# Kernel tuning notes

Hardware: AMD Instinct MI355X
Metric: run time of the kernel (lower is better)

The kernel has to match this reference:

```python
import jax, jax.numpy as jnp
import numpy as np

B, S, D, R = 4, 4096, 1024, 128
EPS_MAG = 1e-8
EPS_LN = 1e-5


def setup_inputs() -> dict:
    key = jax.random.key(0)
    ks = jax.random.split(key, 24)
    w = lambda k, shape, s=0.02: (jax.random.normal(k, shape, jnp.float32) * s)
    d = {}
    d["x"] = jax.random.normal(ks[0], (B, S, D), jnp.float32)
    d["W_dt_down"] = w(ks[1], (D, R))            # dt_proj_down (no bias)
    d["W_dt_up"] = w(ks[2], (R, D))
    d["b_dt_up"] = jnp.full((D,), -4.0, jnp.float32)  # nn.init.constant_(-4.0)
    d["W_gate"] = w(ks[3], (D, D)); d["b_gate"] = jnp.zeros((D,), jnp.float32)
    d["W_phi1"] = w(ks[4], (D, D)); d["b_phi1"] = jnp.zeros((D,), jnp.float32)
    d["W_phi2"] = w(ks[5], (D, D)); d["b_phi2"] = jnp.zeros((D,), jnp.float32)
    d["omega_base"] = jax.random.normal(ks[6], (D,), jnp.float32) * 0.1
    d["W_omega"] = w(ks[7], (D, D)); d["b_omega"] = jnp.zeros((D,), jnp.float32)
    d["W_mag"] = w(ks[8], (D, D)); d["b_mag"] = jnp.zeros((D,), jnp.float32)
    d["W_qoff"] = w(ks[9], (D, D)); d["b_qoff"] = jnp.zeros((D,), jnp.float32)
    d["ln_g"] = jnp.ones((2 * D,), jnp.float32); d["ln_b"] = jnp.zeros((2 * D,), jnp.float32)
    d["W_out1"] = w(ks[10], (2 * D, D)); d["b_out1"] = jnp.zeros((D,), jnp.float32)
    d["W_out2"] = w(ks[11], (D, D)); d["b_out2"] = jnp.zeros((D,), jnp.float32)
    return d


def _forward(x, W_dt_down, W_dt_up, b_dt_up, W_gate, b_gate, W_phi1, b_phi1,
             W_phi2, b_phi2, omega_base, W_omega, b_omega, W_mag, b_mag,
             W_qoff, b_qoff, ln_g, ln_b, W_out1, b_out1, W_out2, b_out2):
    h = x  # expand_factor == 1 -> in_proj is Identity
    # input-dependent delta (low-rank)
    dt = jax.nn.softplus((h @ W_dt_down) @ W_dt_up + b_dt_up)        # [B,S,D]
    select_gate = jax.nn.sigmoid(h @ W_gate + b_gate)
    omega = omega_base + (h @ W_omega + b_omega)
    omega_scaled = omega * dt * 0.01
    phi_init = jax.nn.gelu(h @ W_phi1 + b_phi1, approximate=False) @ W_phi2 + b_phi2
    phi = phi_init + jnp.cumsum(omega_scaled, axis=1)                # phase accumulation
    magnitude = jax.nn.sigmoid(h @ W_mag + b_mag) * 5.0
    content = select_gate * h * magnitude
    memory_real = jnp.cumsum(content * jnp.cos(phi), axis=1)
    memory_imag = jnp.cumsum(content * jnp.sin(phi), axis=1)
    acc_mag = jnp.cumsum(magnitude * select_gate, axis=1)
    sqrt_mag = jnp.sqrt(acc_mag + EPS_MAG)
    mr = memory_real / sqrt_mag
    mi = memory_imag / sqrt_mag
    # rotation-based retrieval
    phi_q = phi + (h @ W_qoff + b_qoff)
    cq, sq = jnp.cos(phi_q), jnp.sin(phi_q)
    retrieved_real = mr * cq + mi * sq
    retrieved_imag = mi * cq - mr * sq
    ctx = jnp.concatenate([retrieved_real, retrieved_imag], axis=-1)  # [B,S,2D]
    mu = jnp.mean(ctx, axis=-1, keepdims=True)
    var = jnp.mean((ctx - mu) ** 2, axis=-1, keepdims=True)
    ln = (ctx - mu) / jnp.sqrt(var + EPS_LN) * ln_g + ln_b
    out = jax.nn.gelu(ln @ W_out1 + b_out1, approximate=False) @ W_out2 + b_out2
    return x + out


def reference(x, W_dt_down, W_dt_up, b_dt_up, W_gate, b_gate, W_phi1, b_phi1,
              W_phi2, b_phi2, omega_base, W_omega, b_omega, W_mag, b_mag,
              W_qoff, b_qoff, ln_g, ln_b, W_out1, b_out1, W_out2, b_out2):
    return _forward(x, W_dt_down, W_dt_up, b_dt_up, W_gate, b_gate, W_phi1, b_phi1,
                    W_phi2, b_phi2, omega_base, W_omega, b_omega, W_mag, b_mag,
                    W_qoff, b_qoff, ln_g, ln_b, W_out1, b_out1, W_out2, b_out2)
```

## Files before the change

### kernel.cpp

```cpp
#include <hip/hip_runtime.h>


#define D_ 1024
#define S_ 4096
#define MH 8192
#define CHUNK 64

typedef float f32x4 __attribute__((ext_vector_type(4)));
typedef __bf16 bf16x8 __attribute__((ext_vector_type(8)));
typedef short s16x8 __attribute__((ext_vector_type(8)));

typedef __attribute__((address_space(1))) void gvoid;
typedef __attribute__((address_space(3))) void lvoid;

__device__ __forceinline__ void g2l16(const void* g, void* l) {
  __builtin_amdgcn_global_load_lds((gvoid*)g, (lvoid*)l, 16, 0, 0);
}

__device__ __forceinline__ float bflo(unsigned int w){ union{unsigned int i; float f;} c; c.i = w<<16; return c.f; }
__device__ __forceinline__ float bfhi(unsigned int w){ union{unsigned int i; float f;} c; c.i = w & 0xFFFF0000u; return c.f; }
__device__ __forceinline__ unsigned short f2bf(float f){
  union{float f; unsigned int i;} c; c.f=f;
  unsigned int u = c.i + 0x7FFFu + ((c.i>>16)&1u);
  return (unsigned short)(u>>16);
}
__device__ __forceinline__ unsigned int pack2(float lo, float hi){
  return (unsigned int)f2bf(lo) | ((unsigned int)f2bf(hi)<<16);
}

__device__ __forceinline__ float sig_(float x){ return 1.f/(1.f+__expf(-x)); }
__device__ __forceinline__ float gelu_(float x){ return 0.5f*x*(1.f+erff(x*0.70710678118654752440f)); }
__device__ __forceinline__ float softplus_(float x){ return (x>0.f) ? x + log1pf(__expf(-x)) : log1pf(__expf(x)); }

template<int EPI, int KK>
__global__ __launch_bounds__(256)
void gemmH(const unsigned short* __restrict__ A,
           const unsigned short* __restrict__ Bt,
           const float* __restrict__ bias,
           const float* __restrict__ extra,
           unsigned short* __restrict__ out0,
           float* __restrict__ outf)
{
  __shared__ unsigned short As[2][128*32];
  __shared__ unsigned short Bs[2][128*32];
  const int tid = threadIdx.x;
  const int m0 = blockIdx.x * 128;
  const int n0 = blockIdx.y * 128;
  const int lane = tid & 63;
  const int wv = tid >> 6;
  const int wr = wv >> 1, wc = wv & 1;
  const int fr = lane & 15, fg = lane >> 4;

  const int r0 = tid >> 2;
  const int k8 = (tid & 3) * 8;

  const unsigned short* ArowA = A  + (size_t)(m0+r0)*KK + k8;
  const unsigned short* ArowB = A  + (size_t)(m0+r0+64)*KK + k8;
  const unsigned short* BrowA = Bt + (size_t)(n0+r0)*KK + k8;
  const unsigned short* BrowB = Bt + (size_t)(n0+r0+64)*KK + k8;

  f32x4 acc[4][4];
#pragma unroll
  for (int i=0;i<4;i++)
#pragma unroll
    for (int j=0;j<4;j++)
#pragma unroll
      for (int q=0;q<4;q++) acc[i][j][q] = 0.f;

  auto STAGE = [&](int buf, int t) {
    const int k0 = t << 5;
    g2l16(ArowA + k0, &As[buf][(size_t)tid*8]);
    g2l16(ArowB + k0, &As[buf][(size_t)(tid+256)*8]);
    g2l16(BrowA + k0, &Bs[buf][(size_t)tid*8]);
    g2l16(BrowB + k0, &Bs[buf][(size_t)(tid+256)*8]);
  };
  auto COMPUTE = [&](int buf) {
    s16x8 af[4], bfr[4];
#pragma unroll
    for (int mf=0; mf<4; mf++) af[mf]  = *(const s16x8*)&As[buf][(wr*64 + mf*16 + fr)*32 + fg*8];
#pragma unroll
    for (int nf=0; nf<4; nf++) bfr[nf] = *(const s16x8*)&Bs[buf][(wc*64 + nf*16 + fr)*32 + fg*8];
#pragma unroll
    for (int mf=0; mf<4; mf++)
#pragma unroll
      for (int nf=0; nf<4; nf++)
        acc[mf][nf] = __builtin_amdgcn_mfma_f32_16x16x32_bf16(
          __builtin_bit_cast(bf16x8, af[mf]), __builtin_bit_cast(bf16x8, bfr[nf]),
          acc[mf][nf], 0, 0, 0);
  };

  const int nt = KK >> 5;
  STAGE(0, 0);
  STAGE(1, 1);
  int cur = 0;
  for (int t = 0; t < nt - 1; ++t) {
    asm volatile("s_waitcnt vmcnt(4)" ::: "memory");
    __builtin_amdgcn_s_barrier();
    __builtin_amdgcn_sched_barrier(0);
    COMPUTE(cur);
    __builtin_amdgcn_s_barrier();
    __builtin_amdgcn_sched_barrier(0);
    if (t + 2 < nt) STAGE(cur, t + 2);
    cur ^= 1;
  }
  asm volatile("s_waitcnt vmcnt(0)" ::: "memory");
  __builtin_amdgcn_s_barrier();
  __builtin_amdgcn_sched_barrier(0);
  COMPUTE(cur);

  const int slice = n0 >> 10;
#pragma unroll
  for (int mf=0; mf<4; mf++) {
#pragma unroll
    for (int nf=0; nf<4; nf++) {
      const int gn = n0 + wc*64 + nf*16 + fr;
      float bv = 0.f;
      if constexpr (EPI != 4) bv = bias[gn];
#pragma unroll
      for (int q=0; q<4; q++) {
        const int gm = m0 + wr*64 + mf*16 + fg*4 + q;
        const float z = acc[mf][nf][q] + bv;
        if constexpr (EPI == 0) {
          const float r = (slice==1) ? sig_(z)*5.f
                        : (slice==3) ? sig_(z)
                        : (slice==4) ? softplus_(z)
                        : (slice==5) ? gelu_(z) : z;
          out0[(size_t)slice*((size_t)MH*1024) + (size_t)gm*1024 + (gn & 1023)] = f2bf(r);
        } else if constexpr (EPI == 1) {
          out0[(size_t)gm*1024 + gn] = f2bf(z);
        } else if constexpr (EPI == 2) {
          out0[(size_t)gm*1024 + gn] = f2bf(gelu_(z));
        } else if constexpr (EPI == 3) {
          const size_t idx = (size_t)gm*1024 + gn;
          outf[idx] = z + extra[idx];
        } else {
          out0[(size_t)gm*1024 + gn] = f2bf(z);
        }
      }
    }
  }
}

__global__ __launch_bounds__(256)
void cvtx_k(const float* __restrict__ x, unsigned int* __restrict__ hb)
{
  const size_t i = (size_t)blockIdx.x*256 + threadIdx.x;
  const float4 v = *(const float4*)(x + i*4);
  hb[i*2]   = pack2(v.x, v.y);
  hb[i*2+1] = pack2(v.z, v.w);
}

__global__ __launch_bounds__(256)
void tconv_k(const float* __restrict__ W, unsigned short* __restrict__ Wt, int K, int N)
{
  __shared__ float tile[32][33];
  const int kb = blockIdx.x*32, nb = blockIdx.y*32;
  const int tx = threadIdx.x & 31, ty = threadIdx.x >> 5;
#pragma unroll
  for (int i=0;i<32;i+=8) tile[ty+i][tx] = W[(size_t)(kb+ty+i)*N + (nb+tx)];
  __syncthreads();
#pragma unroll
  for (int i=0;i<32;i+=8) Wt[(size_t)(nb+ty+i)*K + (kb+tx)] = f2bf(tile[tx][ty+i]);
}

struct P7 { const float* s[7]; unsigned short* d[7]; };
__global__ __launch_bounds__(256)
void tconv7_k(P7 p)
{
  __shared__ float tile[32][33];
  const float* W = p.s[blockIdx.z];
  unsigned short* Wt = p.d[blockIdx.z];
  const int kb = blockIdx.x*32, nb = blockIdx.y*32;
  const int tx = threadIdx.x & 31, ty = threadIdx.x >> 5;
#pragma unroll
  for (int i=0;i<32;i+=8) tile[ty+i][tx] = W[(size_t)(kb+ty+i)*1024 + (nb+tx)];
  __syncthreads();
#pragma unroll
  for (int i=0;i<32;i+=8) Wt[(size_t)(nb+ty+i)*1024 + (kb+tx)] = f2bf(tile[tx][ty+i]);
}

__global__ __launch_bounds__(256)
void biascat_k(const float* bo, const float* ob, const float* bm, const float* bq,
               const float* bg, const float* bdu, const float* bp1, float* bc)
{
  const int i = blockIdx.x*256 + threadIdx.x;
  if (i >= 6144) return;
  const int s = i >> 10, d = i & 1023;
  float v;
  if (s==0) v = bo[d] + ob[d];
  else if (s==1) v = bm[d];
  else if (s==2) v = bq[d];
  else if (s==3) v = bg[d];
  else if (s==4) v = bdu[d];
  else v = bp1[d];
  bc[i] = v;
}

__global__ __launch_bounds__(256)
void scan1_k(unsigned int* __restrict__ zgate, unsigned int* __restrict__ zmag,
             unsigned int* __restrict__ zomega, const unsigned int* __restrict__ zdt,
             const unsigned int* __restrict__ hb,
             float* __restrict__ sumPhi, float* __restrict__ sumGm)
{
  const int flat = blockIdx.x*256 + threadIdx.x;
  const int dh = flat & 511;
  const int bc = flat >> 9;
  size_t i = (size_t)bc*CHUNK*(D_/2) + dh;
  float sp0=0,sp1=0,sg0=0,sg1=0;
  for (int s=0;s<CHUNK;s++,i+=D_/2) {
    const unsigned ga=zgate[i], mg=zmag[i], om=zomega[i], dt=zdt[i], hh=hb[i];
    const float ga0=bflo(ga), ga1=bfhi(ga), mg0=bflo(mg), mg1=bfhi(mg);
    const float od0 = bflo(om)*bflo(dt)*0.01f, od1 = bfhi(om)*bfhi(dt)*0.01f;
    const unsigned odp = pack2(od0, od1);
    zomega[i] = odp;
    sp0 += bflo(odp); sp1 += bfhi(odp);
    const float g0 = ga0*mg0, g1 = ga1*mg1;
    const unsigned gmp = pack2(g0, g1);
    zmag[i] = gmp;
    sg0 += bflo(gmp); sg1 += bfhi(gmp);
    zgate[i] = pack2(g0*bflo(hh), g1*bfhi(hh));
  }
  const int sidx = bc*D_ + dh*2;
  sumPhi[sidx]=sp0; sumPhi[sidx+1]=sp1;
  sumGm[sidx]=sg0;  sumGm[sidx+1]=sg1;
}

__global__ __launch_bounds__(256)
void scan2_k(float* __restrict__ a, float* __restrict__ b)
{
  const int chain = (blockIdx.x*256 + threadIdx.x) >> 6;
  const int lane  = threadIdx.x & 63;
  const int bb = chain >> 10, d = chain & 1023;
  const size_t i = (size_t)(bb*64 + lane)*D_ + d;
  const float v = a[i], w = b[i];
  float vi = v, wi = w;
#pragma unroll
  for (int off=1; off<64; off<<=1) {
    const float t = __shfl_up(vi, off, 64);
    const float u = __shfl_up(wi, off, 64);
    if (lane >= off) { vi += t; wi += u; }
  }
  a[i] = vi - v;
  b[i] = wi - w;
}

__global__ __launch_bounds__(256)
void scan3_k(const unsigned int* __restrict__ omdt, const unsigned int* __restrict__ content,
             const unsigned int* __restrict__ phinit, const float* __restrict__ phiOff,
             float* __restrict__ sumRe, float* __restrict__ sumIm)
{
  const int flat = blockIdx.x*256 + threadIdx.x;
  const int dh = flat & 511;
  const int bc = flat >> 9;
  size_t i = (size_t)bc*CHUNK*(D_/2) + dh;
  const int sidx = bc*D_ + dh*2;
  float p0 = phiOff[sidx], p1 = phiOff[sidx+1];
  float re0=0,re1=0,im0=0,im1=0;
  for (int s=0;s<CHUNK;s++,i+=D_/2) {
    const unsigned od = omdt[i], ct = content[i], pi = phinit[i];
    p0 += bflo(od); p1 += bfhi(od);
    const float phi0 = bflo(pi)+p0, phi1 = bfhi(pi)+p1;
    float s0,c0,s1,c1;
    __sincosf(phi0,&s0,&c0);
    __sincosf(phi1,&s1,&c1);
    const float ct0=bflo(ct), ct1=bfhi(ct);
    re0 += ct0*c0; im0 += ct0*s0;
    re1 += ct1*c1; im1 += ct1*s1;
  }
  sumRe[sidx]=re0; sumRe[sidx+1]=re1;
  sumIm[sidx]=im0; sumIm[sidx+1]=im1;
}

__global__ __launch_bounds__(256)
void scan5_k(const unsigned int* __restrict__ omdt, const unsigned int* __restrict__ content,
             const unsigned int* __restrict__ phinit, const unsigned int* __restrict__ gm,
             const unsigned int* __restrict__ qoff,
             const float* __restrict__ phiOff, const float* __restrict__ gmOff,
             const float* __restrict__ reOff, const float* __restrict__ imOff,
             unsigned int* __restrict__ ctx)
{
  const int flat = blockIdx.x*256 + threadIdx.x;
  const int dh = flat & 511;
  const int bc = flat >> 9;
  size_t i = (size_t)bc*CHUNK*(D_/2) + dh;
  const int sidx = bc*D_ + dh*2;
  float p0 = phiOff[sidx], p1 = phiOff[sidx+1];
  float ag0 = gmOff[sidx], ag1 = gmOff[sidx+1];
  float re0 = reOff[sidx], re1 = reOff[sidx+1];
  float im0 = imOff[sidx], im1 = imOff[sidx+1];
  const int mtok0 = bc*CHUNK;
  for (int s=0;s<CHUNK;s++,i+=D_/2) {
    const unsigned od = omdt[i], ct = content[i], pi = phinit[i], gq = gm[i], qo = qoff[i];
    p0 += bflo(od); p1 += bfhi(od);
    const float phi0 = bflo(pi)+p0, phi1 = bfhi(pi)+p1;
    float sn0,cs0,sn1,cs1;
    __sincosf(phi0,&sn0,&cs0);
    __sincosf(phi1,&sn1,&cs1);
    const float ct0=bflo(ct), ct1=bfhi(ct);
    re0 += ct0*cs0; im0 += ct0*sn0;
    re1 += ct1*cs1; im1 += ct1*sn1;
    ag0 += bflo(gq); ag1 += bfhi(gq);
    const float inv0 = rsqrtf(ag0 + 1e-8f), inv1 = rsqrtf(ag1 + 1e-8f);
    const float mr0 = re0*inv0, mi0 = im0*inv0;
    const float mr1 = re1*inv1, mi1 = im1*inv1;
    const float pq0 = phi0 + bflo(qo), pq1 = phi1 + bfhi(qo);
    float sq0,cq0,sq1,cq1;
    __sincosf(pq0,&sq0,&cq0);
    __sincosf(pq1,&sq1,&cq1);
    const size_t cb = (size_t)(mtok0+s)*D_ + dh;
    ctx[cb]        = pack2(mr0*cq0 + mi0*sq0, mr1*cq1 + mi1*sq1);
    ctx[cb + D_/2] = pack2(mi0*cq0 - mr0*sq0, mi1*cq1 - mr1*sq1);
  }
}

__global__ __launch_bounds__(256)
void ln_k(unsigned int* __restrict__ ctx, const float* __restrict__ gam, const float* __restrict__ bet)
{
  const int m = blockIdx.x, tid = threadIdx.x;
  const size_t base = (size_t)m*1024 + tid*4;
  const uint4 t = *(const uint4*)(ctx + base);
  float v[8] = { bflo(t.x), bfhi(t.x), bflo(t.y), bfhi(t.y),
                 bflo(t.z), bfhi(t.z), bflo(t.w), bfhi(t.w) };
  float s=0.f, ss=0.f;
#pragma unroll
  for (int j=0;j<8;j++){ s+=v[j]; ss+=v[j]*v[j]; }
  for (int o=32;o;o>>=1){ s += __shfl_xor(s,o); ss += __shfl_xor(ss,o); }
  __shared__ float red[8];
  const int wv = tid>>6, lane = tid&63;
  if (lane==0){ red[wv]=s; red[4+wv]=ss; }
  __syncthreads();
  s  = red[0]+red[1]+red[2]+red[3];
  ss = red[4]+red[5]+red[6]+red[7];
  const float mu = s*(1.f/2048.f);
  const float rstd = rsqrtf(ss*(1.f/2048.f) - mu*mu + 1e-5f);
  const int col = tid*8;
  float o[8];
#pragma unroll
  for (int j=0;j<8;j++) o[j] = (v[j]-mu)*rstd*gam[col+j] + bet[col+j];
  uint4 w;
  w.x = pack2(o[0],o[1]); w.y = pack2(o[2],o[3]);
  w.z = pack2(o[4],o[5]); w.w = pack2(o[6],o[7]);
  *(uint4*)(ctx + base) = w;
}

extern "C" void kernel_launch(void* const* d_in, const int* in_sizes, int n_in,
                              void* d_out, int out_size, void* d_ws, size_t ws_size,
                              hipStream_t stream)
{
  const float* x     = (const float*)d_in[0];
  const float* Wdd   = (const float*)d_in[1];
  const float* Wdu   = (const float*)d_in[2];
  const float* bdu   = (const float*)d_in[3];
  const float* Wg    = (const float*)d_in[4];
  const float* bg    = (const float*)d_in[5];
  const float* Wp1   = (const float*)d_in[6];
  const float* bp1   = (const float*)d_in[7];
  const float* Wp2   = (const float*)d_in[8];
  const float* bp2   = (const float*)d_in[9];
  const float* obase = (const float*)d_in[10];
  const float* Wo    = (const float*)d_in[11];
  const float* bo    = (const float*)d_in[12];
  const float* Wm    = (const float*)d_in[13];
  const float* bm    = (const float*)d_in[14];
  const float* Wq    = (const float*)d_in[15];
  const float* bq    = (const float*)d_in[16];
  const float* lng   = (const float*)d_in[17];
  const float* lnb   = (const float*)d_in[18];
  const float* Wo1   = (const float*)d_in[19];
  const float* bo1   = (const float*)d_in[20];
  const float* Wo2   = (const float*)d_in[21];
  const float* bo2   = (const float*)d_in[22];

  char* basep = (char*)d_ws;
  size_t off = 0;
  auto alloc = [&](size_t n) { char* q = basep + off; off = (off + n + 255) & ~(size_t)255; return q; };

  const size_t S = (size_t)MH*1024;
  unsigned short* cat1 = (unsigned short*)alloc(7*S*2);
  unsigned short* zomega = cat1 + 0*S;
  unsigned short* zmag   = cat1 + 1*S;
  unsigned short* zqoff  = cat1 + 2*S;
  unsigned short* zgate  = cat1 + 3*S;
  unsigned short* zdt    = cat1 + 4*S;
  unsigned short* zphi1  = cat1 + 5*S;
  unsigned short* hb     = cat1 + 6*S;
  unsigned short* ctx    = zphi1;
  unsigned short* a3     = cat1;
  unsigned short* zpin   = (unsigned short*)alloc(S*2);
  unsigned short* wt_cat = (unsigned short*)alloc((size_t)6144*1024*2);
  unsigned short* wt_p2  = (unsigned short*)alloc(1024*1024*2);
  unsigned short* wt_du  = (unsigned short*)alloc(1024*128*2);
  unsigned short* wddb   = (unsigned short*)alloc(1024*128*2);
  unsigned short* wt_o1  = (unsigned short*)alloc((size_t)1024*2048*2);
  unsigned short* wt_o2  = (unsigned short*)alloc(1024*1024*2);
  float* bias_cat = (float*)alloc(6144*4);
  float* sumPhi = (float*)alloc((size_t)128*D_*4);
  float* sumGm  = (float*)alloc((size_t)128*D_*4);
  float* sumRe  = (float*)alloc((size_t)128*D_*4);
  float* sumIm  = (float*)alloc((size_t)128*D_*4);

  const dim3 blk(256);

  P7 p7;
  p7.s[0]=Wo;  p7.d[0]=wt_cat + (size_t)0*1024*1024;
  p7.s[1]=Wm;  p7.d[1]=wt_cat + (size_t)1*1024*1024;
  p7.s[2]=Wq;  p7.d[2]=wt_cat + (size_t)2*1024*1024;
  p7.s[3]=Wg;  p7.d[3]=wt_cat + (size_t)3*1024*1024;
  p7.s[4]=Wp1; p7.d[4]=wt_cat + (size_t)5*1024*1024;
  p7.s[5]=Wp2; p7.d[5]=wt_p2;
  p7.s[6]=Wo2; p7.d[6]=wt_o2;
  tconv7_k<<<dim3(32,32,7), blk, 0, stream>>>(p7);
  tconv_k<<<dim3(4,32),  blk, 0, stream>>>(Wdu, wt_du, 128,1024);
  tconv_k<<<dim3(64,32), blk, 0, stream>>>(Wo1, wt_o1, 2048,1024);
  cvtx_k<<<128, blk, 0, stream>>>(Wdd, (unsigned int*)wddb);
  gemmH<4,128><<<dim3(8,8), blk, 0, stream>>>(wt_du, wddb, nullptr, nullptr,
                                              wt_cat + (size_t)4*1024*1024, nullptr);
  biascat_k<<<24, blk, 0, stream>>>(bo, obase, bm, bq, bg, bdu, bp1, bias_cat);

  for (int h = 0; h < 2; h++) {
    const float* xh = x + (size_t)h*MH*D_;
    float* outh     = (float*)d_out + (size_t)h*MH*D_;

    cvtx_k<<<MH*D_/1024, blk, 0, stream>>>(xh, (unsigned int*)hb);

    gemmH<0,1024><<<dim3(MH/128, 48), blk, 0, stream>>>(hb, wt_cat, bias_cat,
                                                        nullptr, cat1, nullptr);
    gemmH<1,1024><<<dim3(MH/128, 8), blk, 0, stream>>>(zphi1, wt_p2, bp2,
                                                       nullptr, zpin, nullptr);
    scan1_k<<<256, blk, 0, stream>>>((unsigned int*)zgate,(unsigned int*)zmag,(unsigned int*)zomega,
                                     (const unsigned int*)zdt,(const unsigned int*)hb, sumPhi, sumGm);
    scan2_k<<<512, blk, 0, stream>>>(sumPhi, sumGm);
    scan3_k<<<256, blk, 0, stream>>>((const unsigned int*)zomega,(const unsigned int*)zgate,
                                     (const unsigned int*)zpin, sumPhi, sumRe, sumIm);
    scan2_k<<<512, blk, 0, stream>>>(sumRe, sumIm);
    scan5_k<<<256, blk, 0, stream>>>((const unsigned int*)zomega,(const unsigned int*)zgate,
                                     (const unsigned int*)zpin,(const unsigned int*)zmag,
                                     (const unsigned int*)zqoff,
                                     sumPhi, sumGm, sumRe, sumIm, (unsigned int*)ctx);

    ln_k<<<MH, blk, 0, stream>>>((unsigned int*)ctx, lng, lnb);
    gemmH<2,2048><<<dim3(MH/128, 8), blk, 0, stream>>>(ctx, wt_o1, bo1,
                                                       nullptr, a3, nullptr);
    gemmH<3,1024><<<dim3(MH/128, 8), blk, 0, stream>>>(a3, wt_o2, bo2,
                                                       xh, nullptr, outh);
  }
}
```

Baseline: 829.8 us.

## Add 256x256-tile 8-wave GEMM with ping-pong schedule for fused input projection

Replaces the 128x128 tiled GEMM for the large concatenated input projection (N=6144) with a new kernel using 256x256 tiles, 512 threads, BK=64, XOR-swizzled LDS, and a barrier-interleaved schedule. The schedule alternates LDS loads and MFMA quadrants under raised priority. The larger tile doubles the arithmetic intensity per global load, and the interleaving is meant to overlap fragment loads with matrix math. The kernel uses 128KB of LDS per block and large accumulators, so only one block fits per CU and the grid is 32x24 blocks. The EPI 0 path is removed from the old kernel.

```diff
diff --git a/kernel.cpp b/kernel.cpp
--- a/kernel.cpp
+++ b/kernel.cpp
@@ -31,6 +31,126 @@
 __device__ __forceinline__ float sig_(float x){ return 1.f/(1.f+__expf(-x)); }
 __device__ __forceinline__ float gelu_(float x){ return 0.5f*x*(1.f+erff(x*0.70710678118654752440f)); }
 __device__ __forceinline__ float softplus_(float x){ return (x>0.f) ? x + log1pf(__expf(-x)) : log1pf(__expf(x)); }
+
+
+#define LDA8(buf, MHH, dst) do { \
+  _Pragma("unroll") for (int f_=0; f_<4; f_++) \
+  _Pragma("unroll") for (int ks_=0; ks_<2; ks_++) \
+    dst[f_][ks_] = *(const s16x8*)&As[buf][(size_t)(wm*128 + (MHH)*64 + f_*16 + fr)*64 + ((ks_*32 + fg*8) ^ swz)]; \
+} while(0)
+
+#define LDB8(buf, NHH, dst) do { \
+  _Pragma("unroll") for (int g_=0; g_<2; g_++) \
+  _Pragma("unroll") for (int ks_=0; ks_<2; ks_++) \
+    dst[g_][ks_] = *(const s16x8*)&Bs[buf][(size_t)(wn*64 + (NHH)*32 + g_*16 + fr)*64 + ((ks_*32 + fg*8) ^ swz)]; \
+} while(0)
+
+#define MMQ8(MHH, NHH, a, b) do { \
+  __builtin_amdgcn_s_setprio(1); \
+  _Pragma("unroll") for (int f_=0; f_<4; f_++) \
+  _Pragma("unroll") for (int g_=0; g_<2; g_++) \
+  _Pragma("unroll") for (int ks_=0; ks_<2; ks_++) \
+    acc[(MHH)*4+f_][(NHH)*2+g_] = __builtin_amdgcn_mfma_f32_16x16x32_bf16( \
+      __builtin_bit_cast(bf16x8, a[f_][ks_]), __builtin_bit_cast(bf16x8, b[g_][ks_]), \
+      acc[(MHH)*4+f_][(NHH)*2+g_], 0, 0, 0); \
+  __builtin_amdgcn_s_setprio(0); \
+} while(0)
+
+#define KTILE8(buf) do { \
+  s16x8 a0_[4][2], a1_[4][2], b0_[2][2], b1_[2][2]; \
+  LDA8(buf, 0, a0_); LDB8(buf, 0, b0_); \
+  __builtin_amdgcn_sched_barrier(0); __builtin_amdgcn_s_barrier(); \
+  MMQ8(0, 0, a0_, b0_); \
+  __builtin_amdgcn_s_barrier(); __builtin_amdgcn_sched_barrier(0); \
+  LDB8(buf, 1, b1_); \
+  __builtin_amdgcn_sched_barrier(0); __builtin_amdgcn_s_barrier(); \
+  MMQ8(0, 1, a0_, b1_); \
+  __builtin_amdgcn_s_barrier(); __builtin_amdgcn_sched_barrier(0); \
+  LDA8(buf, 1, a1_); \
+  __builtin_amdgcn_sched_barrier(0); __builtin_amdgcn_s_barrier(); \
+  MMQ8(1, 1, a1_, b1_); \
+  __builtin_amdgcn_s_barrier(); __builtin_amdgcn_sched_barrier(0); \
+  __builtin_amdgcn_s_barrier(); \
+  MMQ8(1, 0, a1_, b0_); \
+  __builtin_amdgcn_s_barrier(); __builtin_amdgcn_sched_barrier(0); \
+} while(0)
+
+__global__ __launch_bounds__(512)
+void gemm8p(const unsigned short* __restrict__ A,
+            const unsigned short* __restrict__ Bt,
+            const float* __restrict__ bias,
+            unsigned short* __restrict__ out0)
+{
+  __shared__ unsigned short As[2][256*64];
+  __shared__ unsigned short Bs[2][256*64];
+  const int tid = threadIdx.x;
+  const int m0 = blockIdx.x * 256;
+  const int n0 = blockIdx.y * 256;
+  const int lane = tid & 63;
+  const int w  = tid >> 6;
+  const int wm = w >> 2, wn = w & 3;
+  const int fr = lane & 15, fg = lane >> 4;
+  const int swz = (fr & 7) << 3;
+  const int KK = 1024;
+
+  const int srow = tid >> 3;
+  const int csrc = ((tid & 7) ^ (srow & 7)) * 8;
+  const unsigned short* Ag = A  + (size_t)(m0 + srow)*KK + csrc;
+  const unsigned short* Bg = Bt + (size_t)(n0 + srow)*KK + csrc;
+
+  f32x4 acc[8][4];
+#pragma unroll
+  for (int i=0;i<8;i++)
+#pragma unroll
+    for (int j=0;j<4;j++)
+#pragma unroll
+      for (int q=0;q<4;q++) acc[i][j][q] = 0.f;
+
+  auto STAGE = [&](int buf, int t) {
+    const int k0 = t << 6;
+#pragma unroll
+    for (int j = 0; j < 4; j++) {
+      g2l16(Ag + k0 + (size_t)(64*j)*KK, &As[buf][(size_t)tid*8 + 4096*j]);
+      g2l16(Bg + k0 + (size_t)(64*j)*KK, &Bs[buf][(size_t)tid*8 + 4096*j]);
+    }
+  };
+
+  STAGE(0, 0);
+  STAGE(1, 1);
+  for (int i = 0; i < 8; ++i) {
+    asm volatile("s_waitcnt vmcnt(8)" ::: "memory");
+    __builtin_amdgcn_s_barrier();
+    __builtin_amdgcn_sched_barrier(0);
+    KTILE8(0);
+    if (i < 7) STAGE(0, 2*i + 2);
+    if (i < 7) { asm volatile("s_waitcnt vmcnt(8)" ::: "memory"); }
+    else       { asm volatile("s_waitcnt vmcnt(0)" ::: "memory"); }
+    __builtin_amdgcn_s_barrier();
+    __builtin_amdgcn_sched_barrier(0);
+    KTILE8(1);
+    if (i < 7) STAGE(1, 2*i + 3);
+  }
+
+  const int slice = n0 >> 10;
+#pragma unroll
+  for (int mf=0; mf<8; mf++) {
+#pragma unroll
+    for (int nf=0; nf<4; nf++) {
+      const int gn = n0 + wn*64 + nf*16 + fr;
+      const float bv = bias[gn];
+#pragma unroll
+      for (int q=0; q<4; q++) {
+        const int gm = m0 + wm*128 + mf*16 + fg*4 + q;
+        const float z = acc[mf][nf][q] + bv;
+        const float r = (slice==1) ? sig_(z)*5.f
+                      : (slice==3) ? sig_(z)
+                      : (slice==4) ? softplus_(z)
+                      : (slice==5) ? gelu_(z) : z;
+        out0[(size_t)slice*((size_t)MH*1024) + (size_t)gm*1024 + (gn & 1023)] = f2bf(r);
+      }
+    }
+  }
+}
 
 template<int EPI, int KK>
 __global__ __launch_bounds__(256)
@@ -108,7 +228,6 @@
   __builtin_amdgcn_sched_barrier(0);
   COMPUTE(cur);
 
-  const int slice = n0 >> 10;
 #pragma unroll
   for (int mf=0; mf<4; mf++) {
 #pragma unroll
@@ -120,13 +239,7 @@
       for (int q=0; q<4; q++) {
         const int gm = m0 + wr*64 + mf*16 + fg*4 + q;
         const float z = acc[mf][nf][q] + bv;
-        if constexpr (EPI == 0) {
-          const float r = (slice==1) ? sig_(z)*5.f
-                        : (slice==3) ? sig_(z)
-                        : (slice==4) ? softplus_(z)
-                        : (slice==5) ? gelu_(z) : z;
-          out0[(size_t)slice*((size_t)MH*1024) + (size_t)gm*1024 + (gn & 1023)] = f2bf(r);
-        } else if constexpr (EPI == 1) {
+        if constexpr (EPI == 1) {
           out0[(size_t)gm*1024 + gn] = f2bf(z);
         } else if constexpr (EPI == 2) {
           out0[(size_t)gm*1024 + gn] = f2bf(gelu_(z));
@@ -423,8 +536,7 @@
 
     cvtx_k<<<MH*D_/1024, blk, 0, stream>>>(xh, (unsigned int*)hb);
 
-    gemmH<0,1024><<<dim3(MH/128, 48), blk, 0, stream>>>(hb, wt_cat, bias_cat,
-                                                        nullptr, cat1, nullptr);
+    gemm8p<<<dim3(MH/256, 24), dim3(512), 0, stream>>>(hb, wt_cat, bias_cat, cat1);
     gemmH<1,1024><<<dim3(MH/128, 8), blk, 0, stream>>>(zphi1, wt_p2, bp2,
                                                        nullptr, zpin, nullptr);
     scan1_k<<<256, blk, 0, stream>>>((unsigned int*)zgate,(unsigned int*)zmag,(unsigned int*)zomega,
```

Measured after the change: 917.0 us. +10.5%, slower.
